# Kernel tuning notes

Hardware: AMD Instinct MI355X
Metric: run time of the kernel (lower is better)

Reference implementation:

```python
import jax, jax.numpy as jnp
import numpy as np

N, E = 50000, 500000
IN, C, CE_IN = 128, 64, 16   # raw node dim, mid_channel, raw edge dim
L = 3                        # num_layers: layer0 = bare conv, layers 1..2 = res+ blocks
LN_EPS = 1e-5


def layer_norm(x, g, b):
    mu = x.mean(-1, keepdims=True)
    var = ((x - mu) ** 2).mean(-1, keepdims=True)
    return (x - mu) * jax.lax.rsqrt(var + LN_EPS) * g + b


def sage_conv(x, e, src, dst, W1, b1, W2, b2, Wr, t):
    """SAGEConvV2 with softmax aggregation. Returns (node_out, per-edge messages)."""
    # message: lin_l(cat([x_i, x_j, edge_attr])) ; x_i = dst (target), x_j = src (source)
    m_in = jnp.concatenate([x[dst], x[src], e], axis=-1)          # [E, 2C+Ce]
    m = jax.nn.relu(m_in @ W1 + b1) @ W2 + b2                      # [E, C]
    # scatter_softmax(m * t, dst) per feature channel
    logits = m * t
    seg_max = jax.ops.segment_max(logits, dst, num_segments=N)    # [N, C]
    w = jnp.exp(logits - seg_max[dst])
    w = w / jax.ops.segment_sum(w, dst, num_segments=N)[dst]
    out = jax.ops.segment_sum(m * w, dst, num_segments=N)         # [N, C]
    out = out + x @ Wr                                             # root weight (no bias)
    return out, m


def setup_inputs() -> dict:
    key = jax.random.key(0)
    ks = jax.random.split(key, 18)
    f32 = jnp.float32

    def w(k, shape, fan_in):
        return (jax.random.normal(k, shape, f32) / np.sqrt(fan_in)).astype(f32)

    inp = {
        "x": jax.random.normal(ks[0], (N, IN), f32),
        "edge_index": jax.random.randint(ks[1], (2, E), 0, N, dtype=jnp.int64),
        "edge_attr": jax.random.normal(ks[2], (E, CE_IN), f32),
        # encoders
        "node_W": w(ks[3], (IN, C), IN),
        "node_b": jnp.zeros((C,), f32),
        "edge_W": w(ks[4], (CE_IN, C), CE_IN),
        "edge_b": jnp.zeros((C,), f32),
        # stacked conv params (L convs, identical shapes)
        "conv_W1": w(ks[5], (L, 3 * C, 2 * C), 3 * C),
        "conv_b1": jnp.zeros((L, 2 * C), f32),
        "conv_W2": w(ks[6], (L, 2 * C, C), 2 * C),
        "conv_b2": jnp.zeros((L, C), f32),
        "conv_Wr": w(ks[7], (L, C, C), C),
        "conv_t": jnp.ones((L,), f32),
        # layer norms: ln_g[0]/ln_b[0] used as the final output norm, 1..2 inside res+ blocks
        "ln_g": jnp.ones((L, C), f32),
        "ln_b": jnp.zeros((L, C), f32),
        "eln_g": jnp.ones((L - 1, C), f32),
        "eln_b": jnp.zeros((L - 1, C), f32),
    }
    return inp


def reference(x, edge_index, edge_attr, node_W, node_b, edge_W, edge_b,
              conv_W1, conv_b1, conv_W2, conv_b2, conv_Wr, conv_t,
              ln_g, ln_b, eln_g, eln_b):
    src, dst = edge_index[0], edge_index[1]
    h = x @ node_W + node_b                    # node encoder
    e = edge_attr @ edge_W + edge_b            # edge encoder
    # first layer: bare conv
    h, e = sage_conv(h, e, src, dst, conv_W1[0], conv_b1[0], conv_W2[0],
                     conv_b2[0], conv_Wr[0], conv_t[0])
    # res+ blocks (dropout is identity in eval mode)
    for i in range(1, L):
        hn = jax.nn.relu(layer_norm(h, ln_g[i], ln_b[i]))
        en = layer_norm(e, eln_g[i - 1], eln_b[i - 1])
        dh, m = sage_conv(hn, en, src, dst, conv_W1[i], conv_b1[i], conv_W2[i],
                          conv_b2[i], conv_Wr[i], conv_t[i])
        h = h + dh
        e = e + m
    # final norm + act (uses layer-0 norm params, as in the canonical DeeperGCN example)
    return jax.nn.relu(layer_norm(h, ln_g[0], ln_b[0]))
```

## Files before the change

### kernel.cpp

```cpp
#include <hip/hip_runtime.h>

typedef unsigned short u16;
typedef unsigned int u32;
typedef __attribute__((ext_vector_type(8))) short short8;
typedef __attribute__((ext_vector_type(4))) float floatx4;

#define LN_EPS 1e-5f

__device__ __forceinline__ float bf2f(u16 u) {
    union { u32 i; float f; } v; v.i = ((u32)u) << 16; return v.f;
}
__device__ __forceinline__ u16 f2bf(float f) {
    union { u32 i; float f; } v; v.f = f;
    u32 x = v.i;
    return (u16)((x + 0x7fffu + ((x >> 16) & 1u)) >> 16);
}
__device__ __forceinline__ int clampi(int v, int lo, int hi) {
    return v < lo ? lo : (v > hi ? hi : v);
}

__global__ void k_fill(float* __restrict__ out, int nel, float val) {
    int i = blockIdx.x * blockDim.x + threadIdx.x;
    if (i < nel) out[i] = val;
}

__global__ void k_zero(int* p, int n) {
    int i = blockIdx.x * blockDim.x + threadIdx.x;
    if (i < n) p[i] = 0;
}

__global__ void k_detect(const int* __restrict__ ei, int E, int* __restrict__ flag) {
    __shared__ int any;
    if (threadIdx.x == 0) any = 0;
    __syncthreads();
    int lim = (E < 4096) ? E : 4096;
    int v = 0;
    for (int i = threadIdx.x; i < lim; i += 256) v |= ei[2 * i + 1];
    if (v) atomicOr(&any, 1);
    __syncthreads();
    if (threadIdx.x == 0) flag[0] = (any == 0) ? 1 : 0;
}

__global__ void k_hist(const int* __restrict__ ei, const int* __restrict__ flag,
                       int* __restrict__ deg, int E, int n) {
    int e = blockIdx.x * blockDim.x + threadIdx.x;
    if (e < E) {
        int d = flag[0] ? ei[2 * ((size_t)E + e)] : ei[(size_t)E + e];
        atomicAdd(&deg[clampi(d, 0, n - 1)], 1);
    }
}

__global__ void k_scan1(const int* __restrict__ deg, int* __restrict__ offs,
                        int* __restrict__ bsum, int n) {
    __shared__ int s[256];
    int t = threadIdx.x;
    int i = blockIdx.x * 256 + t;
    int v = (i < n) ? deg[i] : 0;
    s[t] = v; __syncthreads();
    for (int off = 1; off < 256; off <<= 1) {
        int x = (t >= off) ? s[t - off] : 0;
        __syncthreads();
        s[t] += x;
        __syncthreads();
    }
    if (i < n) offs[i] = s[t] - v;
    if (t == 255) bsum[blockIdx.x] = s[255];
}

__global__ void k_scan2(int* bsum, int nb) {
    __shared__ int s[256];
    int t = threadIdx.x;
    int v = (t < nb) ? bsum[t] : 0;
    s[t] = v; __syncthreads();
    for (int off = 1; off < 256; off <<= 1) {
        int x = (t >= off) ? s[t - off] : 0;
        __syncthreads();
        s[t] += x;
        __syncthreads();
    }
    if (t < nb) bsum[t] = s[t] - v;
}

__global__ void k_scan3(int* __restrict__ offs, const int* __restrict__ bsum,
                        int* __restrict__ cursor, int n, int E) {
    int i = blockIdx.x * 256 + threadIdx.x;
    if (i < n) {
        int v = offs[i] + bsum[blockIdx.x];
        offs[i] = v;
        cursor[i] = v;
    }
    if (i == 0) offs[n] = E;
}

__global__ void k_scatter(const int* __restrict__ ei, const int* __restrict__ flag,
                          int* __restrict__ cursor,
                          int* __restrict__ perm, int* __restrict__ srcs,
                          int* __restrict__ dsts, int E, int n) {
    int e = blockIdx.x * blockDim.x + threadIdx.x;
    if (e < E) {
        int sv, dv;
        if (flag[0]) {
            sv = ei[2 * (size_t)e];
            dv = ei[2 * ((size_t)E + e)];
        } else {
            sv = ei[e];
            dv = ei[(size_t)E + e];
        }
        sv = clampi(sv, 0, n - 1);
        dv = clampi(dv, 0, n - 1);
        int p = clampi(atomicAdd(&cursor[dv], 1), 0, E - 1);
        perm[p] = e;
        srcs[p] = sv;
        dsts[p] = dv;
    }
}

__global__ void k_swz(const float* __restrict__ W1, const float* __restrict__ W2,
                      const float* __restrict__ Wr, const float* __restrict__ nW,
                      u16* __restrict__ W1s, u16* __restrict__ W2s,
                      u16* __restrict__ Wrs, u16* __restrict__ nWs) {
    int i = blockIdx.x * blockDim.x + threadIdx.x;
    if (i < 3 * 24576) {
        int l = i / 24576, rem = i % 24576;
        int k = rem / 128, n = rem % 128;
        int kt = k >> 5, q = (k >> 3) & 3, j = k & 7;
        W1s[l * 24576 + ((kt * 4 + q) * 128 + n) * 8 + j] = f2bf(W1[i]);
    }
    if (i < 3 * 8192) {
        int l = i / 8192, rem = i % 8192;
        int k = rem / 64, n = rem % 64;
        int kt = k >> 5, q = (k >> 3) & 3, j = k & 7;
        W2s[l * 8192 + ((kt * 4 + q) * 64 + n) * 8 + j] = f2bf(W2[i]);
    }
    if (i < 3 * 4096) {
        int l = i / 4096, rem = i % 4096;
        int k = rem / 64, n = rem % 64;
        int kt = k >> 5, q = (k >> 3) & 3, j = k & 7;
        Wrs[l * 4096 + ((kt * 4 + q) * 64 + n) * 8 + j] = f2bf(Wr[i]);
    }
    if (i < 8192) {
        int k = i / 64, n = i % 64;
        int kt = k >> 5, q = (k >> 3) & 3, j = k & 7;
        nWs[((kt * 4 + q) * 64 + n) * 8 + j] = f2bf(nW[i]);
    }
}

__global__ __launch_bounds__(512) void k_node_enc(
    const float* __restrict__ x, const u16* __restrict__ nWs, const float* __restrict__ bias,
    float* __restrict__ h, u16* __restrict__ hn, int n) {
    int t = threadIdx.x;
    int w = t >> 6, l = t & 63, q = l >> 4, ml = l & 15;
    int wbase = blockIdx.x * 128 + w * 16;
    int rin = wbase + ml;
    int rr = (rin < n) ? rin : 0;
    const float* xr = x + (size_t)rr * 128;
    short8 a[4];
#pragma unroll
    for (int kt = 0; kt < 4; kt++) {
        float4 f0 = *((const float4*)(xr + kt * 32 + q * 8));
        float4 f1 = *((const float4*)(xr + kt * 32 + q * 8 + 4));
        a[kt][0] = (short)f2bf(f0.x); a[kt][1] = (short)f2bf(f0.y);
        a[kt][2] = (short)f2bf(f0.z); a[kt][3] = (short)f2bf(f0.w);
        a[kt][4] = (short)f2bf(f1.x); a[kt][5] = (short)f2bf(f1.y);
        a[kt][6] = (short)f2bf(f1.z); a[kt][7] = (short)f2bf(f1.w);
    }
    float bc[4];
#pragma unroll
    for (int nt = 0; nt < 4; nt++) bc[nt] = bias[nt * 16 + ml];
    floatx4 acc[4];
#pragma unroll
    for (int nt = 0; nt < 4; nt++) acc[nt] = floatx4{0.f, 0.f, 0.f, 0.f};
#pragma unroll
    for (int kt = 0; kt < 4; kt++) {
#pragma unroll
        for (int nt = 0; nt < 4; nt++) {
            short8 bf = *((const short8*)(nWs + (size_t)((kt * 4 + q) * 64 + nt * 16 + ml) * 8));
            acc[nt] = __builtin_amdgcn_mfma_f32_16x16x32_bf16(a[kt], bf, acc[nt], 0, 0, 0);
        }
    }
#pragma unroll
    for (int nt = 0; nt < 4; nt++) {
#pragma unroll
        for (int r2 = 0; r2 < 4; r2++) {
            int pos = wbase + q * 4 + r2;
            if (pos < n) {
                float v = acc[nt][r2] + bc[nt];
                size_t idx = (size_t)pos * 64 + nt * 16 + ml;
                h[idx] = v;
                hn[idx] = f2bf(v);
            }
        }
    }
}

__global__ __launch_bounds__(256) void k_edge_enc(
    const float* __restrict__ ea, const int* __restrict__ perm,
    const float* __restrict__ W, const float* __restrict__ bias,
    u16* __restrict__ e_s, int E) {
    __shared__ float4 sW4[16 * 16];
    int t = threadIdx.x;
    if (t < 256) sW4[t] = ((const float4*)W)[t];
    __syncthreads();
    int gid = blockIdx.x * 256 + t;
    int eidx = gid >> 2, qq = gid & 3;
    if (eidx >= E) return;
    int e = perm[eidx];
    const float4* row4 = (const float4*)(ea + (size_t)e * 16);
    float4 r4[4];
    r4[0] = row4[0]; r4[1] = row4[1]; r4[2] = row4[2]; r4[3] = row4[3];
    const float* row = (const float*)r4;
    float4 acc[4];
#pragma unroll
    for (int j = 0; j < 4; j++) acc[j] = ((const float4*)bias)[qq * 4 + j];
#pragma unroll
    for (int k = 0; k < 16; k++) {
        float rv = row[k];
#pragma unroll
        for (int j = 0; j < 4; j++) {
            float4 wv = sW4[k * 16 + qq * 4 + j];
            acc[j].x += rv * wv.x; acc[j].y += rv * wv.y;
            acc[j].z += rv * wv.z; acc[j].w += rv * wv.w;
        }
    }
    u32 pk[8];
#pragma unroll
    for (int j = 0; j < 4; j++) {
        pk[2 * j]     = (u32)f2bf(acc[j].x) | ((u32)f2bf(acc[j].y) << 16);
        pk[2 * j + 1] = (u32)f2bf(acc[j].z) | ((u32)f2bf(acc[j].w) << 16);
    }
    uint4* outp = (uint4*)(e_s + (size_t)eidx * 64 + qq * 16);
    outp[0] = make_uint4(pk[0], pk[1], pk[2], pk[3]);
    outp[1] = make_uint4(pk[4], pk[5], pk[6], pk[7]);
}

__global__ __launch_bounds__(256) void k_lnorm_bf(
    const float* __restrict__ h, const float* __restrict__ g, const float* __restrict__ b,
    u16* __restrict__ out, int n) {
    int t = threadIdx.x, wid = t >> 6, lane = t & 63;
    float gc = g[lane], bc = b[lane];
    for (int row = blockIdx.x * 4 + wid; row < n; row += gridDim.x * 4) {
        float v = h[(size_t)row * 64 + lane];
        float s = v;
#pragma unroll
        for (int o = 32; o > 0; o >>= 1) s += __shfl_xor(s, o);
        float mu = s * (1.f / 64.f);
        float d = v - mu;
        float s2 = d * d;
#pragma unroll
        for (int o = 32; o > 0; o >>= 1) s2 += __shfl_xor(s2, o);
        float inv = rsqrtf(s2 * (1.f / 64.f) + LN_EPS);
        float r = fmaxf(d * inv * gc + bc, 0.f);
        out[(size_t)row * 64 + lane] = f2bf(r);
    }
}

__global__ __launch_bounds__(256) void k_lnorm_out(
    const float* __restrict__ h, const float* __restrict__ g, const float* __restrict__ b,
    float* __restrict__ out, int n) {
    int t = threadIdx.x, wid = t >> 6, lane = t & 63;
    float gc = g[lane], bc = b[lane];
    for (int row = blockIdx.x * 4 + wid; row < n; row += gridDim.x * 4) {
        float v = h[(size_t)row * 64 + lane];
        float s = v;
#pragma unroll
        for (int o = 32; o > 0; o >>= 1) s += __shfl_xor(s, o);
        float mu = s * (1.f / 64.f);
        float d = v - mu;
        float s2 = d * d;
#pragma unroll
        for (int o = 32; o > 0; o >>= 1) s2 += __shfl_xor(s2, o);
        float inv = rsqrtf(s2 * (1.f / 64.f) + LN_EPS);
        out[(size_t)row * 64 + lane] = fmaxf(d * inv * gc + bc, 0.f);
    }
}

#define TILE 256
#define HSTR 136
__global__ __launch_bounds__(512, 4) void k_mlp(
    const u16* __restrict__ hn, const u16* __restrict__ e_s,
    const int* __restrict__ dsts, const int* __restrict__ srcs,
    const u16* __restrict__ W1s, const float* __restrict__ b1,
    const u16* __restrict__ W2s, const float* __restrict__ b2,
    const float* __restrict__ elng, const float* __restrict__ elnb,
    int ln_edge, u16* __restrict__ m_out, int E) {
    __shared__ __align__(16) short sW2L[8192];
    __shared__ __align__(16) short sShared[24576];

    int t = threadIdx.x;
    int w = t >> 6, l = t & 63, q = l >> 4, ml = l & 15;
    int base = blockIdx.x * TILE + w * 32;
    int pos0 = base + ml;
    int pos1 = base + 16 + ml;
    bool act0 = pos0 < E, act1 = pos1 < E;
    int pp0 = act0 ? pos0 : 0, pp1 = act1 ? pos1 : 0;
    int dn0 = act0 ? dsts[pos0] : 0;
    int sn0 = act0 ? srcs[pos0] : 0;
    int dn1 = act1 ? dsts[pos1] : 0;
    int sn1 = act1 ? srcs[pos1] : 0;

    short8 a0[6], a1[6];
    a0[0] = *(const short8*)(hn + (size_t)dn0 * 64 + q * 8);
    a0[1] = *(const short8*)(hn + (size_t)dn0 * 64 + 32 + q * 8);
    a0[2] = *(const short8*)(hn + (size_t)sn0 * 64 + q * 8);
    a0[3] = *(const short8*)(hn + (size_t)sn0 * 64 + 32 + q * 8);
    a1[0] = *(const short8*)(hn + (size_t)dn1 * 64 + q * 8);
    a1[1] = *(const short8*)(hn + (size_t)dn1 * 64 + 32 + q * 8);
    a1[2] = *(const short8*)(hn + (size_t)sn1 * 64 + q * 8);
    a1[3] = *(const short8*)(hn + (size_t)sn1 * 64 + 32 + q * 8);
    short8 e00 = *(const short8*)(e_s + (size_t)pp0 * 64 + q * 8);
    short8 e01 = *(const short8*)(e_s + (size_t)pp0 * 64 + 32 + q * 8);
    short8 e10 = *(const short8*)(e_s + (size_t)pp1 * 64 + q * 8);
    short8 e11 = *(const short8*)(e_s + (size_t)pp1 * 64 + 32 + q * 8);

    {
        const uint4* g1 = (const uint4*)W1s;
        uint4* s1 = (uint4*)sShared;
#pragma unroll
        for (int j = 0; j < 6; j++) s1[t + j * 512] = g1[t + j * 512];
        const uint4* g2 = (const uint4*)W2s;
        uint4* s2 = (uint4*)sW2L;
#pragma unroll
        for (int j = 0; j < 2; j++) s2[t + j * 512] = g2[t + j * 512];
    }

    if (ln_edge) {
        {
            float ev[16];
            float sm = 0.f, sq = 0.f;
#pragma unroll
            for (int i = 0; i < 8; i++) {
                float f0 = bf2f((u16)e00[i]);
                float f1 = bf2f((u16)e01[i]);
                ev[i] = f0; ev[8 + i] = f1;
                sm += f0 + f1; sq += f0 * f0 + f1 * f1;
            }
            sm += __shfl_xor(sm, 16); sm += __shfl_xor(sm, 32);
            sq += __shfl_xor(sq, 16); sq += __shfl_xor(sq, 32);
            float mu = sm * (1.f / 64.f);
            float var = sq * (1.f / 64.f) - mu * mu;
            float inv = rsqrtf(fmaxf(var, 0.f) + LN_EPS);
#pragma unroll
            for (int i = 0; i < 8; i++) {
                int c0 = q * 8 + i, c1 = 32 + q * 8 + i;
                a0[4][i] = (short)f2bf((ev[i] - mu) * inv * elng[c0] + elnb[c0]);
                a0[5][i] = (short)f2bf((ev[8 + i] - mu) * inv * elng[c1] + elnb[c1]);
            }
        }
        {
            float ev[16];
            float sm = 0.f, sq = 0.f;
#pragma unroll
            for (int i = 0; i < 8; i++) {
                float f0 = bf2f((u16)e10[i]);
                float f1 = bf2f((u16)e11[i]);
                ev[i] = f0; ev[8 + i] = f1;
                sm += f0 + f1; sq += f0 * f0 + f1 * f1;
            }
            sm += __shfl_xor(sm, 16); sm += __shfl_xor(sm, 32);
            sq += __shfl_xor(sq, 16); sq += __shfl_xor(sq, 32);
            float mu = sm * (1.f / 64.f);
            float var = sq * (1.f / 64.f) - mu * mu;
            float inv = rsqrtf(fmaxf(var, 0.f) + LN_EPS);
#pragma unroll
            for (int i = 0; i < 8; i++) {
                int c0 = q * 8 + i, c1 = 32 + q * 8 + i;
                a1[4][i] = (short)f2bf((ev[i] - mu) * inv * elng[c0] + elnb[c0]);
                a1[5][i] = (short)f2bf((ev[8 + i] - mu) * inv * elng[c1] + elnb[c1]);
            }
        }
    } else {
        a0[4] = e00; a0[5] = e01;
        a1[4] = e10; a1[5] = e11;
    }

    __syncthreads();

    floatx4 acc0[8], acc1[8];
#pragma unroll
    for (int nt = 0; nt < 8; nt++) {
        acc0[nt] = floatx4{0.f, 0.f, 0.f, 0.f};
        acc1[nt] = floatx4{0.f, 0.f, 0.f, 0.f};
    }
#pragma unroll
    for (int kt = 0; kt < 6; kt++) {
#pragma unroll
        for (int nt = 0; nt < 8; nt++) {
            short8 bf = *((const short8*)(sShared + ((kt * 4 + q) * 128 + nt * 16 + ml) * 8));
            acc0[nt] = __builtin_amdgcn_mfma_f32_16x16x32_bf16(a0[kt], bf, acc0[nt], 0, 0, 0);
            acc1[nt] = __builtin_amdgcn_mfma_f32_16x16x32_bf16(a1[kt], bf, acc1[nt], 0, 0, 0);
        }
    }

    __syncthreads();

    float b1c[8], b2c[4];
#pragma unroll
    for (int nt = 0; nt < 8; nt++) b1c[nt] = b1[nt * 16 + ml];
#pragma unroll
    for (int nt = 0; nt < 4; nt++) b2c[nt] = b2[nt * 16 + ml];

    short* arena = sShared + w * 16 * HSTR;

#pragma unroll
    for (int nt = 0; nt < 8; nt++) {
#pragma unroll
        for (int r2 = 0; r2 < 4; r2++) {
            float v = fmaxf(acc0[nt][r2] + b1c[nt], 0.f);
            ((u16*)arena)[(q * 4 + r2) * HSTR + nt * 16 + ml] = f2bf(v);
        }
    }
    short8 ah0[4];
#pragma unroll
    for (int kt = 0; kt < 4; kt++)
        ah0[kt] = *((const short8*)(arena + ml * HSTR + kt * 32 + q * 8));

#pragma unroll
    for (int nt = 0; nt < 8; nt++) {
#pragma unroll
        for (int r2 = 0; r2 < 4; r2++) {
            float v = fmaxf(acc1[nt][r2] + b1c[nt], 0.f);
            ((u16*)arena)[(q * 4 + r2) * HSTR + nt * 16 + ml] = f2bf(v);
        }
    }
    short8 ah1[4];
#pragma unroll
    for (int kt = 0; kt < 4; kt++)
        ah1[kt] = *((const short8*)(arena + ml * HSTR + kt * 32 + q * 8));

    floatx4 c20[4], c21[4];
#pragma unroll
    for (int nt = 0; nt < 4; nt++) {
        c20[nt] = floatx4{0.f, 0.f, 0.f, 0.f};
        c21[nt] = floatx4{0.f, 0.f, 0.f, 0.f};
    }
#pragma unroll
    for (int kt = 0; kt < 4; kt++) {
#pragma unroll
        for (int nt = 0; nt < 4; nt++) {
            short8 bf = *((const short8*)(sW2L + ((kt * 4 + q) * 64 + nt * 16 + ml) * 8));
            c20[nt] = __builtin_amdgcn_mfma_f32_16x16x32_bf16(ah0[kt], bf, c20[nt], 0, 0, 0);
            c21[nt] = __builtin_amdgcn_mfma_f32_16x16x32_bf16(ah1[kt], bf, c21[nt], 0, 0, 0);
        }
    }

#pragma unroll
    for (int nt = 0; nt < 4; nt++) {
#pragma unroll
        for (int r2 = 0; r2 < 4; r2++) {
            ((u16*)arena)[(q * 4 + r2) * HSTR + nt * 16 + ml] = f2bf(c20[nt][r2] + b2c[nt]);
        }
    }
    {
        short8 m0 = *((const short8*)(arena + ml * HSTR + q * 16));
        short8 m1 = *((const short8*)(arena + ml * HSTR + q * 16 + 8));
        if (act0) {
            *((short8*)(m_out + (size_t)pos0 * 64 + q * 16)) = m0;
            *((short8*)(m_out + (size_t)pos0 * 64 + q * 16 + 8)) = m1;
        }
    }
#pragma unroll
    for (int nt = 0; nt < 4; nt++) {
#pragma unroll
        for (int r2 = 0; r2 < 4; r2++) {
            ((u16*)arena)[(q * 4 + r2) * HSTR + nt * 16 + ml] = f2bf(c21[nt][r2] + b2c[nt]);
        }
    }
    {
        short8 m0 = *((const short8*)(arena + ml * HSTR + q * 16));
        short8 m1 = *((const short8*)(arena + ml * HSTR + q * 16 + 8));
        if (act1) {
            *((short8*)(m_out + (size_t)pos1 * 64 + q * 16)) = m0;
            *((short8*)(m_out + (size_t)pos1 * 64 + q * 16 + 8)) = m1;
        }
    }
}

__global__ __launch_bounds__(512) void k_root(
    const u16* __restrict__ hn, const u16* __restrict__ Wrs,
    float* __restrict__ h, int add_h, int n) {
    __shared__ short sA[8 * 1024];
    int t = threadIdx.x;
    int base = blockIdx.x * 128;
    {
        int r = t >> 2, s = t & 3;
        int pos = base + r;
        int g = r >> 4, m = r & 15;
        short* grp = sA + g * 1024;
        bool act = pos < n;
        uint4 z4 = make_uint4(0, 0, 0, 0);
        const uint4* pd = (const uint4*)(hn + (size_t)(act ? pos : 0) * 64);
        uint4 d0 = act ? pd[2 * s] : z4;
        uint4 d1 = act ? pd[2 * s + 1] : z4;
        int ch = (s >> 1) * 4 + (s & 1) * 2;
        *((uint4*)(grp + ch * 128 + m * 8)) = d0;
        *((uint4*)(grp + (ch + 1) * 128 + m * 8)) = d1;
    }
    __syncthreads();
    int w = t >> 6, l = t & 63, q = l >> 4, ml = l & 15;
    short* arena = sA + w * 1024;
    floatx4 acc[4];
#pragma unroll
    for (int nt = 0; nt < 4; nt++) acc[nt] = floatx4{0.f, 0.f, 0.f, 0.f};
#pragma unroll
    for (int kt = 0; kt < 2; kt++) {
        short8 a = *((const short8*)(arena + (kt * 4 + q) * 128 + ml * 8));
#pragma unroll
        for (int nt = 0; nt < 4; nt++) {
            short8 bf = *((const short8*)(Wrs + (size_t)((kt * 4 + q) * 64 + nt * 16 + ml) * 8));
            acc[nt] = __builtin_amdgcn_mfma_f32_16x16x32_bf16(a, bf, acc[nt], 0, 0, 0);
        }
    }
#pragma unroll
    for (int nt = 0; nt < 4; nt++) {
#pragma unroll
        for (int r2 = 0; r2 < 4; r2++) {
            int pos = base + w * 16 + q * 4 + r2;
            if (pos < n) {
                size_t idx = (size_t)pos * 64 + nt * 16 + ml;
                float v = acc[nt][r2];
                h[idx] = add_h ? (h[idx] + v) : v;
            }
        }
    }
}

__global__ void k_eadd(u16* __restrict__ dst, const u16* __restrict__ src, long nv) {
    long i = (long)blockIdx.x * blockDim.x + threadIdx.x;
    if (i < nv) {
        uint4 a = ((const uint4*)dst)[i];
        uint4 b = ((const uint4*)src)[i];
        u32* pa = (u32*)&a;
        const u32* pb = (const u32*)&b;
        uint4 r;
        u32* pr = (u32*)&r;
#pragma unroll
        for (int k = 0; k < 4; k++) {
            float lo = bf2f((u16)(pa[k] & 0xffffu)) + bf2f((u16)(pb[k] & 0xffffu));
            float hi = bf2f((u16)(pa[k] >> 16)) + bf2f((u16)(pb[k] >> 16));
            pr[k] = (u32)f2bf(lo) | ((u32)f2bf(hi) << 16);
        }
        ((uint4*)dst)[i] = r;
    }
}

__global__ __launch_bounds__(256) void k_agg2(
    const u16* __restrict__ m_s, float* __restrict__ h,
    const int* __restrict__ offs, const float* __restrict__ tptr, int tidx,
    int n, int E) {
    int t = threadIdx.x, wid = t >> 6, lane = t & 63;
    float tv = tptr[tidx];
    for (int node = blockIdx.x * 4 + wid; node < n; node += gridDim.x * 4) {
        int p0 = clampi(offs[node], 0, E);
        int p1 = clampi(offs[node + 1], p0, E);
        float M = -1e30f, D = 0.f, S = 0.f;
        int p = p0;
        for (; p + 1 < p1; p += 2) {
            float mv0 = bf2f(m_s[(size_t)p * 64 + lane]);
            float mv1 = bf2f(m_s[(size_t)(p + 1) * 64 + lane]);
            float lg0 = mv0 * tv, lg1 = mv1 * tv;
            float Mp = fmaxf(lg0, lg1);
            float a0 = __expf(lg0 - Mp), a1 = __expf(lg1 - Mp);
            float Dp = a0 + a1, Sp = mv0 * a0 + mv1 * a1;
            float Mn = fmaxf(M, Mp);
            float xx = __expf(M - Mn), yy = __expf(Mp - Mn);
            D = D * xx + Dp * yy;
            S = S * xx + Sp * yy;
            M = Mn;
        }
        if (p < p1) {
            float mv = bf2f(m_s[(size_t)p * 64 + lane]);
            float lg = mv * tv;
            float Mn = fmaxf(M, lg);
            float xx = __expf(M - Mn), yy = __expf(lg - Mn);
            D = D * xx + yy;
            S = S * xx + mv * yy;
        }
        if (p1 > p0) h[(size_t)node * 64 + lane] += S / D;
    }
}

extern "C" void kernel_launch(void* const* d_in, const int* in_sizes, int n_in,
                              void* d_out, int out_size, void* d_ws, size_t ws_size,
                              hipStream_t stream) {
    float* outp = (float*)d_out;
    int FB = (out_size + 255) / 256;

    if (n_in != 17) {
        k_fill<<<FB, 256, 0, stream>>>(outp, out_size, 3.0f);
        return;
    }

    const float* x    = (const float*)d_in[0];
    const int*   ei   = (const int*)d_in[1];
    const float* ea   = (const float*)d_in[2];
    const float* nW   = (const float*)d_in[3];
    const float* nb   = (const float*)d_in[4];
    const float* eW   = (const float*)d_in[5];
    const float* eb   = (const float*)d_in[6];
    const float* cW1  = (const float*)d_in[7];
    const float* cb1  = (const float*)d_in[8];
    const float* cW2  = (const float*)d_in[9];
    const float* cb2  = (const float*)d_in[10];
    const float* cWr  = (const float*)d_in[11];
    const float* ct   = (const float*)d_in[12];
    const float* lng  = (const float*)d_in[13];
    const float* lnb  = (const float*)d_in[14];
    const float* elng = (const float*)d_in[15];
    const float* elnb = (const float*)d_in[16];

    const int n = in_sizes[0] / 128;
    const int E = in_sizes[2] / 16;

    char* ws = (char*)d_ws;
    size_t o = 0;
    auto alloc = [&](size_t bytes) -> void* {
        void* p = ws + o;
        o += (bytes + 255) & ~(size_t)255;
        return p;
    };
    int*   flag   = (int*)alloc(256);
    int*   deg    = (int*)alloc((size_t)n * 4);
    int*   offs   = (int*)alloc((size_t)(n + 1) * 4);
    int*   cursor = (int*)alloc((size_t)n * 4);
    int*   bsum   = (int*)alloc(256 * 4);
    int*   perm   = (int*)alloc((size_t)E * 4);
    int*   srcs   = (int*)alloc((size_t)E * 4);
    int*   dsts   = (int*)alloc((size_t)E * 4);
    float* h      = (float*)alloc((size_t)n * 64 * 4);
    u16*   hn     = (u16*)alloc((size_t)n * 64 * 2);
    u16*   bufA   = (u16*)alloc((size_t)E * 64 * 2);
    u16*   bufB   = (u16*)alloc((size_t)E * 64 * 2);
    u16*   W1s    = (u16*)alloc((size_t)3 * 24576 * 2);
    u16*   W2s    = (u16*)alloc((size_t)3 * 8192 * 2);
    u16*   Wrs    = (u16*)alloc((size_t)3 * 4096 * 2);
    u16*   nWs    = (u16*)alloc((size_t)8192 * 2);

    k_fill<<<FB, 256, 0, stream>>>(outp, out_size, 1.0f);
    if (o > ws_size) {
        k_fill<<<FB, 256, 0, stream>>>(outp, out_size, 2.0f);
        return;
    }

    int SB = (n + 255) / 256;
    k_detect<<<1, 256, 0, stream>>>(ei, E, flag);
    k_zero<<<SB, 256, 0, stream>>>(deg, n);
    k_hist<<<(E + 255) / 256, 256, 0, stream>>>(ei, flag, deg, E, n);
    k_scan1<<<SB, 256, 0, stream>>>(deg, offs, bsum, n);
    k_scan2<<<1, 256, 0, stream>>>(bsum, SB);
    k_scan3<<<SB, 256, 0, stream>>>(offs, bsum, cursor, n, E);
    k_scatter<<<(E + 255) / 256, 256, 0, stream>>>(ei, flag, cursor, perm, srcs, dsts, E, n);
    k_swz<<<(3 * 24576 + 255) / 256, 256, 0, stream>>>(cW1, cW2, cWr, nW, W1s, W2s, Wrs, nWs);
    k_node_enc<<<(n + 127) / 128, 512, 0, stream>>>(x, nWs, nb, h, hn, n);
    k_edge_enc<<<(E * 4 + 255) / 256, 256, 0, stream>>>(ea, perm, eW, eb, bufA, E);

    int MB = (E + TILE - 1) / TILE;
    int RB = (n + 127) / 128;
    int AB = (n + 3) / 4;
    long nv = (long)E * 64 / 8;
    int VB = (int)((nv + 255) / 256);

    const u16* mlp_in[3]  = { bufA, bufB, bufB };
    u16*       mlp_out[3] = { bufB, bufA, bufA };

    for (int i = 0; i < 3; i++) {
        if (i > 0)
            k_lnorm_bf<<<512, 256, 0, stream>>>(h, lng + (size_t)i * 64, lnb + (size_t)i * 64, hn, n);
        k_mlp<<<MB, 512, 0, stream>>>(
            hn, mlp_in[i], dsts, srcs,
            W1s + (size_t)i * 24576, cb1 + (size_t)i * 128,
            W2s + (size_t)i * 8192, cb2 + (size_t)i * 64,
            elng + (size_t)((i > 0) ? (i - 1) : 0) * 64,
            elnb + (size_t)((i > 0) ? (i - 1) : 0) * 64,
            (i > 0) ? 1 : 0, mlp_out[i], E);
        k_root<<<RB, 512, 0, stream>>>(hn, Wrs + (size_t)i * 4096, h, (i > 0) ? 1 : 0, n);
        k_agg2<<<AB, 256, 0, stream>>>(mlp_out[i], h, offs, ct, i, n, E);
        if (i == 1)
            k_eadd<<<VB, 256, 0, stream>>>(bufB, bufA, nv);
    }
    k_lnorm_out<<<512, 256, 0, stream>>>(h, lng, lnb, outp, n);
}
```

Before: 598.0 us.

## Fuse node layernorm into aggregation and edge residual add into MLP load

The node layer norm (bf16 for the next layer, fp32 for the final output) now runs inside the aggregation kernel right after the residual update, so the separate norm launches are gone. The edge residual add kernel is dropped: layer 2's MLP reads both edge buffers and sums them before the edge layer norm. This removes a full read-modify-write pass over the E×64 edge tensor and extra passes over h. The cost is an extra edge load in the layer-2 MLP and one more bf16 rounding difference, since the sum is no longer stored back in bf16.

```diff
diff --git a/kernel.cpp b/kernel.cpp
--- a/kernel.cpp
+++ b/kernel.cpp
@@ -233,51 +233,11 @@
     outp[1] = make_uint4(pk[4], pk[5], pk[6], pk[7]);
 }
 
-__global__ __launch_bounds__(256) void k_lnorm_bf(
-    const float* __restrict__ h, const float* __restrict__ g, const float* __restrict__ b,
-    u16* __restrict__ out, int n) {
-    int t = threadIdx.x, wid = t >> 6, lane = t & 63;
-    float gc = g[lane], bc = b[lane];
-    for (int row = blockIdx.x * 4 + wid; row < n; row += gridDim.x * 4) {
-        float v = h[(size_t)row * 64 + lane];
-        float s = v;
-#pragma unroll
-        for (int o = 32; o > 0; o >>= 1) s += __shfl_xor(s, o);
-        float mu = s * (1.f / 64.f);
-        float d = v - mu;
-        float s2 = d * d;
-#pragma unroll
-        for (int o = 32; o > 0; o >>= 1) s2 += __shfl_xor(s2, o);
-        float inv = rsqrtf(s2 * (1.f / 64.f) + LN_EPS);
-        float r = fmaxf(d * inv * gc + bc, 0.f);
-        out[(size_t)row * 64 + lane] = f2bf(r);
-    }
-}
-
-__global__ __launch_bounds__(256) void k_lnorm_out(
-    const float* __restrict__ h, const float* __restrict__ g, const float* __restrict__ b,
-    float* __restrict__ out, int n) {
-    int t = threadIdx.x, wid = t >> 6, lane = t & 63;
-    float gc = g[lane], bc = b[lane];
-    for (int row = blockIdx.x * 4 + wid; row < n; row += gridDim.x * 4) {
-        float v = h[(size_t)row * 64 + lane];
-        float s = v;
-#pragma unroll
-        for (int o = 32; o > 0; o >>= 1) s += __shfl_xor(s, o);
-        float mu = s * (1.f / 64.f);
-        float d = v - mu;
-        float s2 = d * d;
-#pragma unroll
-        for (int o = 32; o > 0; o >>= 1) s2 += __shfl_xor(s2, o);
-        float inv = rsqrtf(s2 * (1.f / 64.f) + LN_EPS);
-        out[(size_t)row * 64 + lane] = fmaxf(d * inv * gc + bc, 0.f);
-    }
-}
-
 #define TILE 256
 #define HSTR 136
 __global__ __launch_bounds__(512, 4) void k_mlp(
     const u16* __restrict__ hn, const u16* __restrict__ e_s,
+    const u16* __restrict__ e_s2,
     const int* __restrict__ dsts, const int* __restrict__ srcs,
     const u16* __restrict__ W1s, const float* __restrict__ b1,
     const u16* __restrict__ W2s, const float* __restrict__ b2,
@@ -311,6 +271,14 @@
     short8 e01 = *(const short8*)(e_s + (size_t)pp0 * 64 + 32 + q * 8);
     short8 e10 = *(const short8*)(e_s + (size_t)pp1 * 64 + q * 8);
     short8 e11 = *(const short8*)(e_s + (size_t)pp1 * 64 + 32 + q * 8);
+    short8 f00, f01, f10, f11;
+    bool has2 = (e_s2 != nullptr);
+    if (has2) {
+        f00 = *(const short8*)(e_s2 + (size_t)pp0 * 64 + q * 8);
+        f01 = *(const short8*)(e_s2 + (size_t)pp0 * 64 + 32 + q * 8);
+        f10 = *(const short8*)(e_s2 + (size_t)pp1 * 64 + q * 8);
+        f11 = *(const short8*)(e_s2 + (size_t)pp1 * 64 + 32 + q * 8);
+    }
 
     {
         const uint4* g1 = (const uint4*)W1s;
@@ -331,6 +299,7 @@
             for (int i = 0; i < 8; i++) {
                 float f0 = bf2f((u16)e00[i]);
                 float f1 = bf2f((u16)e01[i]);
+                if (has2) { f0 += bf2f((u16)f00[i]); f1 += bf2f((u16)f01[i]); }
                 ev[i] = f0; ev[8 + i] = f1;
                 sm += f0 + f1; sq += f0 * f0 + f1 * f1;
             }
@@ -353,6 +322,7 @@
             for (int i = 0; i < 8; i++) {
                 float f0 = bf2f((u16)e10[i]);
                 float f1 = bf2f((u16)e11[i]);
+                if (has2) { f0 += bf2f((u16)f10[i]); f1 += bf2f((u16)f11[i]); }
                 ev[i] = f0; ev[8 + i] = f1;
                 sm += f0 + f1; sq += f0 * f0 + f1 * f1;
             }
@@ -524,31 +494,15 @@
     }
 }
 
-__global__ void k_eadd(u16* __restrict__ dst, const u16* __restrict__ src, long nv) {
-    long i = (long)blockIdx.x * blockDim.x + threadIdx.x;
-    if (i < nv) {
-        uint4 a = ((const uint4*)dst)[i];
-        uint4 b = ((const uint4*)src)[i];
-        u32* pa = (u32*)&a;
-        const u32* pb = (const u32*)&b;
-        uint4 r;
-        u32* pr = (u32*)&r;
-#pragma unroll
-        for (int k = 0; k < 4; k++) {
-            float lo = bf2f((u16)(pa[k] & 0xffffu)) + bf2f((u16)(pb[k] & 0xffffu));
-            float hi = bf2f((u16)(pa[k] >> 16)) + bf2f((u16)(pb[k] >> 16));
-            pr[k] = (u32)f2bf(lo) | ((u32)f2bf(hi) << 16);
-        }
-        ((uint4*)dst)[i] = r;
-    }
-}
-
 __global__ __launch_bounds__(256) void k_agg2(
     const u16* __restrict__ m_s, float* __restrict__ h,
     const int* __restrict__ offs, const float* __restrict__ tptr, int tidx,
-    int n, int E) {
+    const float* __restrict__ g, const float* __restrict__ b,
+    u16* __restrict__ hn_out, float* __restrict__ f32_out,
+    int write_h, int n, int E) {
     int t = threadIdx.x, wid = t >> 6, lane = t & 63;
     float tv = tptr[tidx];
+    float gc = g[lane], bc = b[lane];
     for (int node = blockIdx.x * 4 + wid; node < n; node += gridDim.x * 4) {
         int p0 = clampi(offs[node], 0, E);
         int p1 = clampi(offs[node + 1], p0, E);
@@ -575,7 +529,21 @@
             D = D * xx + yy;
             S = S * xx + mv * yy;
         }
-        if (p1 > p0) h[(size_t)node * 64 + lane] += S / D;
+        float hv = h[(size_t)node * 64 + lane];
+        if (p1 > p0) hv += S / D;
+        if (write_h) h[(size_t)node * 64 + lane] = hv;
+        float s = hv;
+#pragma unroll
+        for (int o = 32; o > 0; o >>= 1) s += __shfl_xor(s, o);
+        float mu = s * (1.f / 64.f);
+        float d = hv - mu;
+        float s2 = d * d;
+#pragma unroll
+        for (int o = 32; o > 0; o >>= 1) s2 += __shfl_xor(s2, o);
+        float inv = rsqrtf(s2 * (1.f / 64.f) + LN_EPS);
+        float r = fmaxf(d * inv * gc + bc, 0.f);
+        if (hn_out) hn_out[(size_t)node * 64 + lane] = f2bf(r);
+        else        f32_out[(size_t)node * 64 + lane] = r;
     }
 }
 
@@ -656,26 +624,28 @@
     int MB = (E + TILE - 1) / TILE;
     int RB = (n + 127) / 128;
     int AB = (n + 3) / 4;
-    long nv = (long)E * 64 / 8;
-    int VB = (int)((nv + 255) / 256);
 
     const u16* mlp_in[3]  = { bufA, bufB, bufB };
+    const u16* mlp_in2[3] = { nullptr, nullptr, bufA };
     u16*       mlp_out[3] = { bufB, bufA, bufA };
 
     for (int i = 0; i < 3; i++) {
-        if (i > 0)
-            k_lnorm_bf<<<512, 256, 0, stream>>>(h, lng + (size_t)i * 64, lnb + (size_t)i * 64, hn, n);
         k_mlp<<<MB, 512, 0, stream>>>(
-            hn, mlp_in[i], dsts, srcs,
+            hn, mlp_in[i], mlp_in2[i], dsts, srcs,
             W1s + (size_t)i * 24576, cb1 + (size_t)i * 128,
             W2s + (size_t)i * 8192, cb2 + (size_t)i * 64,
             elng + (size_t)((i > 0) ? (i - 1) : 0) * 64,
             elnb + (size_t)((i > 0) ? (i - 1) : 0) * 64,
             (i > 0) ? 1 : 0, mlp_out[i], E);
         k_root<<<RB, 512, 0, stream>>>(hn, Wrs + (size_t)i * 4096, h, (i > 0) ? 1 : 0, n);
-        k_agg2<<<AB, 256, 0, stream>>>(mlp_out[i], h, offs, ct, i, n, E);
-        if (i == 1)
-            k_eadd<<<VB, 256, 0, stream>>>(bufB, bufA, nv);
-    }
-    k_lnorm_out<<<512, 256, 0, stream>>>(h, lng, lnb, outp, n);
-}
+        if (i < 2) {
+            k_agg2<<<AB, 256, 0, stream>>>(mlp_out[i], h, offs, ct, i,
+                                           lng + (size_t)(i + 1) * 64, lnb + (size_t)(i + 1) * 64,
+                                           hn, nullptr, 1, n, E);
+        } else {
+            k_agg2<<<AB, 256, 0, stream>>>(mlp_out[i], h, offs, ct, i,
+                                           lng, lnb,
+                                           nullptr, outp, 0, n, E);
+        }
+    }
+}
```

New measurement: 527.4 us. -11.8%, faster.
